# Optimization experiments

Measured on AMD Instinct MI355X. Metric: run time of the kernel, lower is better.

Reference implementation:

```python
import jax, jax.numpy as jnp
import numpy as np

NUM_FIELDS = 40
EMBED_DIM = 64
ATTN_DIM = 32

def _triu_index(n):
    i, j = np.triu_indices(n, k=1)
    return jnp.asarray(i, jnp.int32), jnp.asarray(j, jnp.int32)

def setup_inputs() -> dict:
    key = jax.random.key(0)
    k0, k1, k2, k3, k4, k5 = jax.random.split(key, 6)
    B = 8192
    inputs = jax.random.normal(k0, (B, NUM_FIELDS, EMBED_DIM), dtype=jnp.float32)
    # attention MLP params (PyTorch Linear default init scale ~ 1/sqrt(fan_in))
    s1 = 1.0 / np.sqrt(EMBED_DIM)
    s2 = 1.0 / np.sqrt(ATTN_DIM)
    W1 = jax.random.uniform(k1, (EMBED_DIM, ATTN_DIM), jnp.float32, -s1, s1)
    b1 = jax.random.uniform(k2, (ATTN_DIM,), jnp.float32, -s1, s1)
    w2 = jax.random.uniform(k3, (ATTN_DIM,), jnp.float32, -s2, s2)
    p = jax.random.uniform(k4, (EMBED_DIM,), jnp.float32, -s1, s1)
    return {"inputs": inputs, "W1": W1, "b1": b1, "w2": w2, "p": p}

def reference(inputs, W1, b1, w2, p):
    idx0, idx1 = _triu_index(NUM_FIELDS)  # [P], P = 780 pairs
    # gather pairwise field embeddings and take elementwise product: [B, P, D]
    prod = inputs[:, idx0, :] * inputs[:, idx1, :]
    # tiny attention MLP: Linear -> ReLU -> Linear(no bias) -> softmax over pairs
    h = jax.nn.relu(jnp.einsum('bpd,da->bpa', prod, W1) + b1)  # [B, P, A]
    logits = jnp.einsum('bpa,a->bp', h, w2)                    # [B, P]
    attn = jax.nn.softmax(logits, axis=1)                      # softmax over pair dim
    # attention-weighted sum pooling over pairs: [B, D]
    pooled = jnp.einsum('bp,bpd->bd', attn, prod)
    # final linear projection to scalar (dropout=0 / eval -> identity)
    return jnp.einsum('bd,d->b', pooled, p)
```

## Files before the change

kernel.cpp:

```cpp
#include <hip/hip_runtime.h>


typedef _Float16 f16;
typedef f16 f16x8 __attribute__((ext_vector_type(8)));
typedef f16 f16x4 __attribute__((ext_vector_type(4)));
typedef f16 f16x2 __attribute__((ext_vector_type(2)));
typedef float fx16 __attribute__((ext_vector_type(16)));

#define NF 40
#define DD 64
#define NB 8192

__global__ __launch_bounds__(256, 2) void afm_kernel(
    const float* __restrict__ x,
    const float* __restrict__ W1,
    const float* __restrict__ b1,
    const float* __restrict__ w2,
    const float* __restrict__ p,
    float* __restrict__ out)
{
    __shared__ f16 xh[4][64 * 64];

    const int wid  = threadIdx.x >> 6;
    const int lane = threadIdx.x & 63;
    const int b    = blockIdx.x * 4 + wid;
    f16* Xs = &xh[wid][0];

    const float4* xb = (const float4*)(x + (size_t)b * (NF * DD));
#pragma unroll
    for (int t = 0; t < 10; ++t) {
        int idx = t * 64 + lane;
        float4 v = xb[idx];
        f16x4 h;
        h.x = (f16)v.x; h.y = (f16)v.y; h.z = (f16)v.z; h.w = (f16)v.w;
        *(f16x4*)(Xs + idx * 4) = h;
    }
    f16x4 z = {};
#pragma unroll
    for (int t = 0; t < 6; ++t) {
        int idx = 640 + t * 64 + lane;
        *(f16x4*)(Xs + idx * 4) = z;
    }
    __syncthreads();

    const int nl = lane & 31;
    const int hh = lane >> 5;
    const int h8 = hh * 8;

    f16x8 w1f[4];
#pragma unroll
    for (int kt = 0; kt < 4; ++kt)
#pragma unroll
        for (int j = 0; j < 8; ++j)
            w1f[kt][j] = (f16)W1[(kt * 16 + h8 + j) * 32 + nl];

    f16x2 pp[4][4];
#pragma unroll
    for (int kt = 0; kt < 4; ++kt)
#pragma unroll
        for (int j2 = 0; j2 < 4; ++j2) {
            pp[kt][j2].x = (f16)p[kt * 16 + h8 + 2 * j2];
            pp[kt][j2].y = (f16)p[kt * 16 + h8 + 2 * j2 + 1];
        }

    float b1v[16], w2v[16];
#pragma unroll
    for (int r = 0; r < 16; ++r) {
        int a = (r & 3) + 8 * (r >> 2) + 4 * hh;
        b1v[r] = b1[a];
        w2v[r] = w2[a];
    }

    float accW = 0.f, accWS = 0.f;

#pragma unroll
    for (int ig = 0; ig < 2; ++ig) {
        const int i = ig * 32 + nl;
        f16x8 xif[4];
#pragma unroll
        for (int kt = 0; kt < 4; ++kt)
            xif[kt] = *(const f16x8*)(Xs + i * 64 + kt * 16 + h8);

        const int j0 = ig * 32 + 1;
        for (int j = j0; j < NF; ++j) {
            fx16 C;
#pragma unroll
            for (int r = 0; r < 16; ++r) C[r] = b1v[r];
            float sp = 0.f;
#pragma unroll
            for (int kt = 0; kt < 4; ++kt) {
                f16x8 xj = *(const f16x8*)(Xs + j * 64 + kt * 16 + h8);
                f16x8 pr = xif[kt] * xj;
                f16x2 t0; t0.x = pr[0]; t0.y = pr[1];
                f16x2 t1; t1.x = pr[2]; t1.y = pr[3];
                f16x2 t2; t2.x = pr[4]; t2.y = pr[5];
                f16x2 t3; t3.x = pr[6]; t3.y = pr[7];
                sp = __builtin_amdgcn_fdot2(t0, pp[kt][0], sp, false);
                sp = __builtin_amdgcn_fdot2(t1, pp[kt][1], sp, false);
                sp = __builtin_amdgcn_fdot2(t2, pp[kt][2], sp, false);
                sp = __builtin_amdgcn_fdot2(t3, pp[kt][3], sp, false);
                C = __builtin_amdgcn_mfma_f32_32x32x16_f16(w1f[kt], pr, C, 0, 0, 0);
            }
            float l = 0.f;
#pragma unroll
            for (int r = 0; r < 16; ++r) {
                float hv = fmaxf(C[r], 0.f);
                l = fmaf(hv, w2v[r], l);
            }
            l  += __shfl_xor(l, 32);
            sp += __shfl_xor(sp, 32);
            bool valid = (i < j);
            float w = valid ? __expf(l) : 0.f;
            accW += w;
            accWS = fmaf(w, sp, accWS);
        }
    }

#pragma unroll
    for (int m = 16; m >= 1; m >>= 1) {
        accW  += __shfl_xor(accW, m);
        accWS += __shfl_xor(accWS, m);
    }
    if (lane == 0) out[b] = accWS / accW;
}

extern "C" void kernel_launch(void* const* d_in, const int* in_sizes, int n_in,
                              void* d_out, int out_size, void* d_ws, size_t ws_size,
                              hipStream_t stream) {
    const float* x  = (const float*)d_in[0];
    const float* W1 = (const float*)d_in[1];
    const float* b1 = (const float*)d_in[2];
    const float* w2 = (const float*)d_in[3];
    const float* p  = (const float*)d_in[4];
    float* out = (float*)d_out;
    dim3 grid(NB / 4), block(256);
    hipLaunchKernelGGL(afm_kernel, grid, block, 0, stream, x, W1, b1, w2, p, out);
}
```

Before: 184.5 us.

## Remap pair enumeration to cut wasted MFMA iterations, pad LDS rows

Replaces the two-pass i-group loop, which computed many invalid (i>=j) pairs, with a cyclic enumeration over the first 32 fields (16 rotations), then 8 iterations pairing those fields with fields 32-39, and a single pass that covers the 28 pairs among fields 32-39 by inverting a triangular index. The goal is fewer MFMA iterations per batch row. It also pads shared-memory rows to a stride of 76 halves to reduce bank conflicts, drops the zero-fill of unused rows, and raises launch bounds to 4 waves per SIMD. The added index arithmetic (sqrt-based triangular inversion) and the smaller register budget could offset some of the gain.

```diff
diff --git a/kernel.cpp b/kernel.cpp
--- a/kernel.cpp
+++ b/kernel.cpp
@@ -2,16 +2,18 @@
 
 
 typedef _Float16 f16;
+typedef f16 f16x2 __attribute__((ext_vector_type(2)));
+typedef f16 f16x4 __attribute__((ext_vector_type(4)));
 typedef f16 f16x8 __attribute__((ext_vector_type(8)));
-typedef f16 f16x4 __attribute__((ext_vector_type(4)));
-typedef f16 f16x2 __attribute__((ext_vector_type(2)));
 typedef float fx16 __attribute__((ext_vector_type(16)));
 
 #define NF 40
-#define DD 64
 #define NB 8192
+#define STR 76
 
-__global__ __launch_bounds__(256, 2) void afm_kernel(
+union V8 { f16x8 v8; f16x4 v4[2]; f16x2 v2[4]; };
+
+__global__ __launch_bounds__(256, 4) void afm_kernel(
     const float* __restrict__ x,
     const float* __restrict__ W1,
     const float* __restrict__ b1,
@@ -19,27 +21,22 @@
     const float* __restrict__ p,
     float* __restrict__ out)
 {
-    __shared__ f16 xh[4][64 * 64];
+    __shared__ f16 xh[4][NF * STR];
 
     const int wid  = threadIdx.x >> 6;
     const int lane = threadIdx.x & 63;
     const int b    = blockIdx.x * 4 + wid;
     f16* Xs = &xh[wid][0];
 
-    const float4* xb = (const float4*)(x + (size_t)b * (NF * DD));
+    const float4* xb = (const float4*)(x + (size_t)b * (NF * 64));
 #pragma unroll
     for (int t = 0; t < 10; ++t) {
         int idx = t * 64 + lane;
         float4 v = xb[idx];
-        f16x4 h;
-        h.x = (f16)v.x; h.y = (f16)v.y; h.z = (f16)v.z; h.w = (f16)v.w;
-        *(f16x4*)(Xs + idx * 4) = h;
-    }
-    f16x4 z = {};
-#pragma unroll
-    for (int t = 0; t < 6; ++t) {
-        int idx = 640 + t * 64 + lane;
-        *(f16x4*)(Xs + idx * 4) = z;
+        f16x4 h = { (f16)v.x, (f16)v.y, (f16)v.z, (f16)v.w };
+        int r = idx >> 4;
+        int d = (idx & 15) * 4;
+        *(f16x4*)(Xs + r * STR + d) = h;
     }
     __syncthreads();
 
@@ -47,73 +44,97 @@
     const int hh = lane >> 5;
     const int h8 = hh * 8;
 
-    f16x8 w1f[4];
+    V8 w1f[4];
 #pragma unroll
     for (int kt = 0; kt < 4; ++kt)
 #pragma unroll
         for (int j = 0; j < 8; ++j)
-            w1f[kt][j] = (f16)W1[(kt * 16 + h8 + j) * 32 + nl];
+            w1f[kt].v8[j] = (f16)W1[(kt * 16 + h8 + j) * 32 + nl];
 
-    f16x2 pp[4][4];
+    f16x2 pp[16];
 #pragma unroll
     for (int kt = 0; kt < 4; ++kt)
 #pragma unroll
-        for (int j2 = 0; j2 < 4; ++j2) {
-            pp[kt][j2].x = (f16)p[kt * 16 + h8 + 2 * j2];
-            pp[kt][j2].y = (f16)p[kt * 16 + h8 + 2 * j2 + 1];
+        for (int m = 0; m < 4; ++m) {
+            f16x2 t2 = { (f16)p[kt * 16 + h8 + 2 * m], (f16)p[kt * 16 + h8 + 2 * m + 1] };
+            pp[kt * 4 + m] = t2;
         }
 
-    float b1v[16], w2v[16];
+    fx16 b1C;
+    float w2v[16];
 #pragma unroll
     for (int r = 0; r < 16; ++r) {
         int a = (r & 3) + 8 * (r >> 2) + 4 * hh;
-        b1v[r] = b1[a];
+        b1C[r] = b1[a];
         w2v[r] = w2[a];
+    }
+
+    f16x4 xif[8];
+#pragma unroll
+    for (int kt = 0; kt < 4; ++kt) {
+        const f16* src = Xs + nl * STR + kt * 16 + h8;
+        xif[2 * kt]     = *(const f16x4*)(src);
+        xif[2 * kt + 1] = *(const f16x4*)(src + 4);
     }
 
     float accW = 0.f, accWS = 0.f;
 
+    auto body = [&](const f16x4* xi, int jrow, bool valid) {
+        const f16* base = Xs + jrow * STR + h8;
+        V8 pr[4];
 #pragma unroll
-    for (int ig = 0; ig < 2; ++ig) {
-        const int i = ig * 32 + nl;
-        f16x8 xif[4];
+        for (int kt = 0; kt < 4; ++kt) {
+            f16x4 a0 = *(const f16x4*)(base + kt * 16);
+            f16x4 a1 = *(const f16x4*)(base + kt * 16 + 4);
+            pr[kt].v4[0] = xi[2 * kt] * a0;
+            pr[kt].v4[1] = xi[2 * kt + 1] * a1;
+        }
+        fx16 C = __builtin_amdgcn_mfma_f32_32x32x16_f16(w1f[0].v8, pr[0].v8, b1C, 0, 0, 0);
+        C = __builtin_amdgcn_mfma_f32_32x32x16_f16(w1f[1].v8, pr[1].v8, C, 0, 0, 0);
+        C = __builtin_amdgcn_mfma_f32_32x32x16_f16(w1f[2].v8, pr[2].v8, C, 0, 0, 0);
+        C = __builtin_amdgcn_mfma_f32_32x32x16_f16(w1f[3].v8, pr[3].v8, C, 0, 0, 0);
+        float sp = 0.f;
 #pragma unroll
         for (int kt = 0; kt < 4; ++kt)
-            xif[kt] = *(const f16x8*)(Xs + i * 64 + kt * 16 + h8);
+#pragma unroll
+            for (int m = 0; m < 4; ++m)
+                sp = __builtin_amdgcn_fdot2(pr[kt].v2[m], pp[kt * 4 + m], sp, false);
+        float l0 = 0.f, l1 = 0.f;
+#pragma unroll
+        for (int r = 0; r < 8; ++r) {
+            l0 = fmaf(fmaxf(C[2 * r], 0.f),     w2v[2 * r],     l0);
+            l1 = fmaf(fmaxf(C[2 * r + 1], 0.f), w2v[2 * r + 1], l1);
+        }
+        float l = l0 + l1;
+        l  += __shfl_xor(l, 32);
+        sp += __shfl_xor(sp, 32);
+        float w = valid ? __expf(l) : 0.f;
+        accW += w;
+        accWS = fmaf(w, sp, accWS);
+    };
 
-        const int j0 = ig * 32 + 1;
-        for (int j = j0; j < NF; ++j) {
-            fx16 C;
+    for (int t = 1; t <= 16; ++t)
+        body(xif, (nl + t) & 31, (t < 16) | (nl < 16));
+
+    for (int u = 0; u < 8; ++u)
+        body(xif, 32 + u, true);
+
+    {
+        int q = nl < 28 ? nl : 27;
+        float disc = 225.0f - 8.0f * (float)q;
+        int ii = (int)((15.0f - sqrtf(disc)) * 0.5f);
+        if (ii * (15 - ii) / 2 > q) --ii;
+        if ((ii + 1) * (14 - ii) / 2 <= q) ++ii;
+        int jj = q - ii * (15 - ii) / 2 + ii + 1;
+        int iC = 32 + ii, jC = 32 + jj;
+        f16x4 xi2[8];
 #pragma unroll
-            for (int r = 0; r < 16; ++r) C[r] = b1v[r];
-            float sp = 0.f;
-#pragma unroll
-            for (int kt = 0; kt < 4; ++kt) {
-                f16x8 xj = *(const f16x8*)(Xs + j * 64 + kt * 16 + h8);
-                f16x8 pr = xif[kt] * xj;
-                f16x2 t0; t0.x = pr[0]; t0.y = pr[1];
-                f16x2 t1; t1.x = pr[2]; t1.y = pr[3];
-                f16x2 t2; t2.x = pr[4]; t2.y = pr[5];
-                f16x2 t3; t3.x = pr[6]; t3.y = pr[7];
-                sp = __builtin_amdgcn_fdot2(t0, pp[kt][0], sp, false);
-                sp = __builtin_amdgcn_fdot2(t1, pp[kt][1], sp, false);
-                sp = __builtin_amdgcn_fdot2(t2, pp[kt][2], sp, false);
-                sp = __builtin_amdgcn_fdot2(t3, pp[kt][3], sp, false);
-                C = __builtin_amdgcn_mfma_f32_32x32x16_f16(w1f[kt], pr, C, 0, 0, 0);
-            }
-            float l = 0.f;
-#pragma unroll
-            for (int r = 0; r < 16; ++r) {
-                float hv = fmaxf(C[r], 0.f);
-                l = fmaf(hv, w2v[r], l);
-            }
-            l  += __shfl_xor(l, 32);
-            sp += __shfl_xor(sp, 32);
-            bool valid = (i < j);
-            float w = valid ? __expf(l) : 0.f;
-            accW += w;
-            accWS = fmaf(w, sp, accWS);
+        for (int kt = 0; kt < 4; ++kt) {
+            const f16* src = Xs + iC * STR + kt * 16 + h8;
+            xi2[2 * kt]     = *(const f16x4*)(src);
+            xi2[2 * kt + 1] = *(const f16x4*)(src + 4);
         }
+        body(xi2, jC, nl < 28);
     }
 
 #pragma unroll
```

Result: faster. 153.0 us (-17.1%).
